# Performance work log

Hardware: AMD Instinct MI355X
Metric: run time of the kernel (lower is better)

The kernel has to match this reference:

```python
import jax, jax.numpy as jnp
import numpy as np

H = 32          # query heads
HKV = 8         # kv heads
HD = 128        # head dim
BS = 64         # sparse block size
LOCAL = 16      # local blocks
VERT = 8        # vertical stride
STEP = 1        # head sliding step = max(1, VERT // H) for non-homo heads
BASE = 1000000.0
ROPE_SCALE = 1.0
SCALE = 1.0 / np.sqrt(HD)


def setup_inputs() -> dict:
    key = jax.random.key(0)
    ks = jax.random.split(key, 6)
    T, D = 2048, H * HD
    std = 0.02
    return {
        'hidden_states': jax.random.normal(ks[0], (T, D), jnp.float32),
        'positions': jnp.arange(T, dtype=jnp.int32),
        'Wq': jax.random.normal(ks[1], (D, H * HD), jnp.float32) * std,
        'bq': jnp.zeros((H * HD,), jnp.float32),
        'Wk': jax.random.normal(ks[2], (D, HKV * HD), jnp.float32) * std,
        'bk': jnp.zeros((HKV * HD,), jnp.float32),
        'Wv': jax.random.normal(ks[3], (D, HKV * HD), jnp.float32) * std,
        'bv': jnp.zeros((HKV * HD,), jnp.float32),
        'Wo': jax.random.normal(ks[4], (D, D), jnp.float32) * std,
        'bo': jnp.zeros((D,), jnp.float32),
    }


def _rope_cos_sin(positions):
    # neox-style rotary, linear scaling (factor 1.0 -> identity)
    inv_freq = 1.0 / (BASE ** (jnp.arange(0, HD, 2, dtype=jnp.float32) / HD))  # [HD/2]
    t = positions.astype(jnp.float32) / ROPE_SCALE                             # [T]
    freqs = t[:, None] * inv_freq[None, :]                                     # [T, HD/2]
    return jnp.cos(freqs), jnp.sin(freqs)


def _apply_rope(x, cos, sin):
    # x: [T, h, HD], neox: rotate halves
    x1, x2 = x[..., : HD // 2], x[..., HD // 2 :]
    c, s = cos[:, None, :], sin[:, None, :]
    return jnp.concatenate([x1 * c - x2 * s, x2 * c + x1 * s], axis=-1)


def _block_sparse_mask(T):
    # per-head local + vertical-stride block pattern, causal at token level
    blk = jnp.arange(T) // BS
    qb, kb = blk[:, None], blk[None, :]                      # [T,T] block ids
    heads = jnp.arange(H)
    local = (qb - kb) < LOCAL                                # [T,T]
    vert = ((kb[None, :, :] + heads[:, None, None] * STEP + 1) % VERT) == 0  # [H,T,T]
    causal = jnp.arange(T)[:, None] >= jnp.arange(T)[None, :]
    return causal[None] & (local[None] | vert)               # [H,T,T] bool


def reference(hidden_states, positions, Wq, bq, Wk, bk, Wv, bv, Wo, bo):
    T = hidden_states.shape[0]
    q = (hidden_states @ Wq + bq).reshape(T, H, HD)
    k = (hidden_states @ Wk + bk).reshape(T, HKV, HD)
    v = (hidden_states @ Wv + bv).reshape(T, HKV, HD)

    cos, sin = _rope_cos_sin(positions)
    q = _apply_rope(q, cos, sin)
    k = _apply_rope(k, cos, sin)

    # GQA: repeat kv heads to match query heads
    k = jnp.repeat(k, H // HKV, axis=1)   # [T,H,HD]
    v = jnp.repeat(v, H // HKV, axis=1)

    scores = jnp.einsum('shd,thd->hst', q, k) * SCALE         # [H,T,T]
    mask = _block_sparse_mask(T)
    scores = jnp.where(mask, scores, jnp.finfo(scores.dtype).min)
    probs = jax.nn.softmax(scores, axis=-1)
    out = jnp.einsum('hst,thd->shd', probs, v).reshape(T, H * HD)
    return out @ Wo + bo
```

## Files before the change

kernel.cpp:

```cpp
#include <hip/hip_runtime.h>
#include <type_traits>

#define H_    32
#define HKV_  8
#define HD_   128
#define D_    4096
#define KVD_  1024
#define NQKV_ 6144

typedef __attribute__((ext_vector_type(8))) short s8v;
typedef __attribute__((ext_vector_type(4))) float f4v;

__device__ __forceinline__ float b2f(unsigned short u) {
  union { unsigned int i; float f; } v; v.i = ((unsigned int)u) << 16; return v.f;
}
__device__ __forceinline__ unsigned short f2b(float f) {
  unsigned int u = __float_as_uint(f);
  u += 0x7fffu + ((u >> 16) & 1u);
  return (unsigned short)(u >> 16);
}

__device__ __forceinline__ void gload16(const unsigned short* g, unsigned short* l) {
  __builtin_amdgcn_global_load_lds((const __attribute__((address_space(1))) void*)g,
                                   (__attribute__((address_space(3))) void*)l, 16, 0, 0);
}

__global__ void cvt_bf16(const float* __restrict__ x, unsigned short* __restrict__ y,
                         int n8)
{
  int i = blockIdx.x * blockDim.x + threadIdx.x;
  if (i >= n8) return;
  const float4* xp = (const float4*)x + (size_t)i * 2;
  float4 a = xp[0], b = xp[1];
  s8v v;
  v[0] = (short)f2b(a.x); v[1] = (short)f2b(a.y);
  v[2] = (short)f2b(a.z); v[3] = (short)f2b(a.w);
  v[4] = (short)f2b(b.x); v[5] = (short)f2b(b.y);
  v[6] = (short)f2b(b.z); v[7] = (short)f2b(b.w);
  *(s8v*)(y + (size_t)i * 8) = v;
}

__global__ void concat_bias(const float* __restrict__ bq, const float* __restrict__ bk,
                            const float* __restrict__ bv, float* __restrict__ o)
{
  int i = blockIdx.x * blockDim.x + threadIdx.x;
  float v = (i < D_) ? bq[i] : (i < D_ + KVD_) ? bk[i - D_] : bv[i - D_ - KVD_];
  o[i] = v;
}

__global__ __launch_bounds__(256) void cvt_transpose(
    const float* __restrict__ W, unsigned short* __restrict__ Wt, int K, int N)
{
  __shared__ unsigned short tile[64][72];
  const int k0 = blockIdx.y * 64, n0 = blockIdx.x * 64;
  const int tid = threadIdx.x;
#pragma unroll
  for (int it = 0; it < 4; ++it) {
    int idx = tid + it * 256;
    int r = idx >> 4;
    int c = (idx & 15) << 2;
    float4 w = *(const float4*)(W + (size_t)(k0 + r) * N + n0 + c);
    tile[c + 0][r] = f2b(w.x); tile[c + 1][r] = f2b(w.y);
    tile[c + 2][r] = f2b(w.z); tile[c + 3][r] = f2b(w.w);
  }
  __syncthreads();
#pragma unroll
  for (int it = 0; it < 2; ++it) {
    int idx = tid + it * 256;
    int n = idx >> 3;
    int kk = (idx & 7) << 3;
    *(s8v*)(Wt + (size_t)(n0 + n) * K + k0 + kk) = *(const s8v*)&tile[n][kk];
  }
}

__global__ __launch_bounds__(256) void vtrans(
    const unsigned short* __restrict__ S, int lds_, unsigned short* __restrict__ Dst,
    int T)
{
  __shared__ unsigned short tile[64][72];
  const int v0 = blockIdx.x * 64, t0 = blockIdx.y * 64;
  const int tid = threadIdx.x;
#pragma unroll
  for (int it = 0; it < 2; ++it) {
    int idx = tid + it * 256;
    int tr = idx >> 3;
    int vc = (idx & 7) << 3;
    s8v val = *(const s8v*)(S + (size_t)(t0 + tr) * lds_ + v0 + vc);
#pragma unroll
    for (int u = 0; u < 8; ++u) tile[vc + u][tr] = (unsigned short)val[u];
  }
  __syncthreads();
#pragma unroll
  for (int it = 0; it < 2; ++it) {
    int idx = tid + it * 256;
    int vr = idx >> 3;
    int tc = (idx & 7) << 3;
    *(s8v*)(Dst + (size_t)(v0 + vr) * T + t0 + tc) = *(const s8v*)&tile[vr][tc];
  }
}

template <typename OT>
__global__ __launch_bounds__(512, 2) void gemm_bt4p(
    const unsigned short* __restrict__ A, const unsigned short* __restrict__ Bt,
    const float* __restrict__ bias, OT* __restrict__ C,
    int M, int N, int K, int ldc)
{
  __shared__ __align__(16) unsigned short lds[65536];

  const int tid  = threadIdx.x;
  const int wave = tid >> 6;
  const int lane = tid & 63;
  const int l16  = lane & 15;
  const int quad = lane >> 4;
  const int wm   = wave >> 2;
  const int wn   = wave & 3;

  const int nbx = N >> 8;
  const int nwg = nbx * (M >> 8);
  int bid = blockIdx.x;
  if ((nwg & 7) == 0) bid = (bid & 7) * (nwg >> 3) + (bid >> 3);
  const int row0 = (bid / nbx) << 8;
  const int col0 = (bid % nbx) << 8;

  const int srow = lane >> 2;
  const int scol = (((lane & 3) ^ ((lane >> 3) & 3)) << 3);
  const unsigned short* ApL = A  + (size_t)(row0 + wave * 32 + srow) * K + scol;
  const unsigned short* BpL = Bt + (size_t)(col0 + wave * 32 + srow) * K + scol;

  unsigned short* ldsA = lds;
  unsigned short* ldsB = lds + 32768;
  const int wst = wave * 1024;

  const int sl = ((quad ^ ((l16 >> 1) & 3)) << 3);
  const int arow = wm * 128 + l16;
  const int brow = wn * 64 + l16;

  f4v acc[8][4] = {};
  const int nt = K >> 6;

  {
    const unsigned short* sa = ApL;
    const unsigned short* sb = BpL;
    gload16(sa,                       ldsA + wst);
    gload16(sa + 16 * (size_t)K,      ldsA + wst + 512);
    gload16(sb,                       ldsB + wst);
    gload16(sb + 16 * (size_t)K,      ldsB + wst + 512);
    gload16(sa + 32,                  ldsA + 8192 + wst);
    gload16(sa + 32 + 16 * (size_t)K, ldsA + 8192 + wst + 512);
    gload16(sb + 32,                  ldsB + 8192 + wst);
    gload16(sb + 32 + 16 * (size_t)K, ldsB + 8192 + wst + 512);
  }
  asm volatile("s_waitcnt vmcnt(4)" ::: "memory");
  asm volatile("s_barrier" ::: "memory");

  for (int t = 0; t < nt; ++t) {
    const int p = t & 1;
    const unsigned short* Ab0 = ldsA + p * 16384;
    const unsigned short* Ab1 = Ab0 + 8192;
    const unsigned short* Bb0 = ldsB + p * 16384;
    const unsigned short* Bb1 = Bb0 + 8192;
    unsigned short* An = ldsA + (p ^ 1) * 16384;
    unsigned short* Bn = ldsB + (p ^ 1) * 16384;
    const bool pre = (t + 1 < nt);
    const unsigned short* sa = ApL + (size_t)(t + 1) * 64;
    const unsigned short* sb = BpL + (size_t)(t + 1) * 64;

    s8v a[8], b0, b1, b2, b3;

    b0 = *(const s8v*)&Bb0[(brow +  0) * 32 + sl];
    b1 = *(const s8v*)&Bb0[(brow + 16) * 32 + sl];
#pragma unroll
    for (int i = 0; i < 8; ++i)
      a[i] = *(const s8v*)&Ab0[(arow + i * 16) * 32 + sl];
    if (pre) {
      gload16(sa,                  An + wst);
      gload16(sa + 16 * (size_t)K, An + wst + 512);
    }
    __builtin_amdgcn_s_setprio(1);
#pragma unroll
    for (int i = 0; i < 8; ++i) {
      acc[i][0] = __builtin_amdgcn_mfma_f32_16x16x32_bf16(a[i], b0, acc[i][0], 0, 0, 0);
      acc[i][1] = __builtin_amdgcn_mfma_f32_16x16x32_bf16(a[i], b1, acc[i][1], 0, 0, 0);
    }
    __builtin_amdgcn_s_setprio(0);

    b2 = *(const s8v*)&Bb0[(brow + 32) * 32 + sl];
    b3 = *(const s8v*)&Bb0[(brow + 48) * 32 + sl];
    if (pre) {
      gload16(sb,                  Bn + wst);
      gload16(sb + 16 * (size_t)K, Bn + wst + 512);
      asm volatile("s_waitcnt vmcnt(4)" ::: "memory");
    } else {
      asm volatile("s_waitcnt vmcnt(0)" ::: "memory");
    }
    asm volatile("s_barrier" ::: "memory");
    __builtin_amdgcn_s_setprio(1);
#pragma unroll
    for (int i = 0; i < 8; ++i) {
      acc[i][2] = __builtin_amdgcn_mfma_f32_16x16x32_bf16(a[i], b2, acc[i][2], 0, 0, 0);
      acc[i][3] = __builtin_amdgcn_mfma_f32_16x16x32_bf16(a[i], b3, acc[i][3], 0, 0, 0);
    }
    __builtin_amdgcn_s_setprio(0);

    b2 = *(const s8v*)&Bb1[(brow + 32) * 32 + sl];
    b3 = *(const s8v*)&Bb1[(brow + 48) * 32 + sl];
#pragma unroll
    for (int i = 0; i < 8; ++i)
      a[i] = *(const s8v*)&Ab1[(arow + i * 16) * 32 + sl];
    if (pre) {
      gload16(sa + 32,                  An + 8192 + wst);
      gload16(sa + 32 + 16 * (size_t)K, An + 8192 + wst + 512);
    }
    __builtin_amdgcn_s_setprio(1);
#pragma unroll
    for (int i = 0; i < 8; ++i) {
      acc[i][2] = __builtin_amdgcn_mfma_f32_16x16x32_bf16(a[i], b2, acc[i][2], 0, 0, 0);
      acc[i][3] = __builtin_amdgcn_mfma_f32_16x16x32_bf16(a[i], b3, acc[i][3], 0, 0, 0);
    }
    __builtin_amdgcn_s_setprio(0);

    b0 = *(const s8v*)&Bb1[(brow +  0) * 32 + sl];
    b1 = *(const s8v*)&Bb1[(brow + 16) * 32 + sl];
    if (pre) {
      gload16(sb + 32,                  Bn + 8192 + wst);
      gload16(sb + 32 + 16 * (size_t)K, Bn + 8192 + wst + 512);
      asm volatile("s_waitcnt vmcnt(4)" ::: "memory");
    }
    asm volatile("s_barrier" ::: "memory");
    __builtin_amdgcn_s_setprio(1);
#pragma unroll
    for (int i = 0; i < 8; ++i) {
      acc[i][0] = __builtin_amdgcn_mfma_f32_16x16x32_bf16(a[i], b0, acc[i][0], 0, 0, 0);
      acc[i][1] = __builtin_amdgcn_mfma_f32_16x16x32_bf16(a[i], b1, acc[i][1], 0, 0, 0);
    }
    __builtin_amdgcn_s_setprio(0);
  }

#pragma unroll
  for (int j = 0; j < 4; ++j) {
    const int col = col0 + wn * 64 + j * 16 + l16;
    const float bc = bias[col];
#pragma unroll
    for (int i = 0; i < 8; ++i) {
      const int rowb = row0 + wm * 128 + i * 16 + quad * 4;
#pragma unroll
      for (int r = 0; r < 4; ++r) {
        float o = acc[i][j][r] + bc;
        if constexpr (std::is_same_v<OT, float>) C[(size_t)(rowb + r) * ldc + col] = o;
        else                                     C[(size_t)(rowb + r) * ldc + col] = f2b(o);
      }
    }
  }
}

__global__ void sincos_tab(const int* __restrict__ pos, float* __restrict__ ct,
                           float* __restrict__ st)
{
  const int t = blockIdx.x, d = threadIdx.x;
  float inv = powf(1.0e6f, -(float)d * (1.0f / 64.0f));
  float fr  = (float)pos[t] * inv;
  float s, c;
  sincosf(fr, &s, &c);
  ct[t * 64 + d] = c;
  st[t * 64 + d] = s;
}

__global__ void rope_apply(unsigned short* __restrict__ qkv,
                           const float* __restrict__ ct, const float* __restrict__ st,
                           int T)
{
  const int t  = blockIdx.x;
  const int hh = blockIdx.y;
  const int d  = threadIdx.x;
  unsigned short* p = qkv + (size_t)t * NQKV_ + hh * HD_;
  const float g = (hh < H_) ? (0.08838834764831845f * 1.4426950408889634f) : 1.0f;
  float c = ct[t * 64 + d], s = st[t * 64 + d];
  float x1 = b2f(p[d]), x2 = b2f(p[d + 64]);
  p[d]      = f2b((x1 * c - x2 * s) * g);
  p[d + 64] = f2b((x2 * c + x1 * s) * g);
}

__global__ __launch_bounds__(256) void attn_sparse(
    const unsigned short* __restrict__ QKV, int ldq,
    const unsigned short* __restrict__ Vt, unsigned short* __restrict__ O, int T)
{
  __shared__ __align__(16) unsigned short lds[16384];
  unsigned short* ldsK = lds;
  unsigned short* ldsV = lds + 8192;
  unsigned short* ldsP = lds;

  const int h    = blockIdx.x;
  const int qb   = (gridDim.y - 1) - blockIdx.y;
  const int hkv  = h >> 2;
  const int tid  = threadIdx.x;
  const int wave = tid >> 6;
  const int lane = tid & 63;
  const int l16  = lane & 15;
  const int quad = lane >> 4;

  const int qrow = qb * 64 + wave * 16 + l16;
  s8v qf[4];
#pragma unroll
  for (int s = 0; s < 4; ++s)
    qf[s] = *(const s8v*)(QKV + (size_t)qrow * ldq + h * HD_ + s * 32 + quad * 8);

  const int lr4 = lane >> 2;
  const int lc8 = (lane & 3) << 3;
  const unsigned short* Kp0 = QKV + (size_t)(wave * 16 + lr4) * ldq
                              + D_ + hkv * HD_ + lc8;
  unsigned short* Kd0 = ldsK + wave * 512;
  const unsigned short* Vp0 = Vt + (size_t)(hkv * HD_ + wave * 32 + lr4) * T + lc8;
  unsigned short* Vd0 = ldsV + wave * 1024;

  float mrow[4] = {-1e30f, -1e30f, -1e30f, -1e30f};
  float lrow[4] = {0.f, 0.f, 0.f, 0.f};
  f4v oacc[8] = {};
  const int rowinb = wave * 16 + quad * 4;

  for (int kb = 0; kb <= qb; ++kb) {
    if (!((qb - kb < 16) || (((kb + h + 1) & 7) == 0))) continue;

    __syncthreads();
    {
      const unsigned short* kp = Kp0 + (size_t)(kb * 64) * ldq;
      const unsigned short* vp = Vp0 + kb * 64;
#pragma unroll
      for (int t = 0; t < 4; ++t)
        gload16(kp + t * 32, Kd0 + t * 2048);
#pragma unroll
      for (int t = 0; t < 4; ++t)
        gload16(vp + (size_t)((t >> 1) * 16) * T + (t & 1) * 32,
                Vd0 + (t & 1) * 4096 + (t >> 1) * 512);
    }
    __syncthreads();

    f4v sacc[4] = {};
#pragma unroll
    for (int kt = 0; kt < 4; ++kt) {
#pragma unroll
      for (int s = 0; s < 4; ++s) {
        s8v b = *(const s8v*)&ldsK[s * 2048 + (kt * 16 + l16) * 32 + quad * 8];
        sacc[kt] = __builtin_amdgcn_mfma_f32_16x16x32_bf16(qf[s], b, sacc[kt], 0, 0, 0);
      }
    }
    __syncthreads();

    const bool diag = (kb == qb);
    float p[4][4];
#pragma unroll
    for (int r = 0; r < 4; ++r) {
      float mx = -1e30f;
#pragma unroll
      for (int kt = 0; kt < 4; ++kt) {
        float sc = sacc[kt][r];
        if (diag && (kt * 16 + l16 > rowinb + r)) sc = -1e30f;
        p[r][kt] = sc;
        mx = fmaxf(mx, sc);
      }
#pragma unroll
      for (int off = 1; off < 16; off <<= 1)
        mx = fmaxf(mx, __shfl_xor(mx, off));
      float newm = fmaxf(mrow[r], mx);
      float alpha = exp2f(mrow[r] - newm);
      mrow[r] = newm;
      float rs = 0.f;
#pragma unroll
      for (int kt = 0; kt < 4; ++kt) {
        unsigned short pb = f2b(exp2f(p[r][kt] - newm));
        ldsP[wave * 1152 + (quad * 4 + r) * 72 + kt * 16 + l16] = pb;
        rs += b2f(pb);
      }
#pragma unroll
      for (int off = 1; off < 16; off <<= 1)
        rs += __shfl_xor(rs, off);
      lrow[r] = lrow[r] * alpha + rs;
#pragma unroll
      for (int dt = 0; dt < 8; ++dt) oacc[dt][r] *= alpha;
    }

#pragma unroll
    for (int s2 = 0; s2 < 2; ++s2) {
      s8v af = *(const s8v*)&ldsP[wave * 1152 + l16 * 72 + s2 * 32 + quad * 8];
#pragma unroll
      for (int dt = 0; dt < 8; ++dt) {
        s8v vf = *(const s8v*)&ldsV[s2 * 4096 + (dt * 16 + l16) * 32 + quad * 8];
        oacc[dt] = __builtin_amdgcn_mfma_f32_16x16x32_bf16(af, vf, oacc[dt], 0, 0, 0);
      }
    }
  }

#pragma unroll
  for (int r = 0; r < 4; ++r) {
    float inv = 1.0f / lrow[r];
    size_t rowoff = (size_t)(qb * 64 + rowinb + r) * D_ + h * HD_;
#pragma unroll
    for (int dt = 0; dt < 8; ++dt)
      O[rowoff + dt * 16 + l16] = f2b(oacc[dt][r] * inv);
  }
}

extern "C" void kernel_launch(void* const* d_in, const int* in_sizes, int n_in,
                              void* d_out, int out_size, void* d_ws, size_t ws_size,
                              hipStream_t stream)
{
  const float* hs  = (const float*)d_in[0];
  const int*   pos = (const int*)d_in[1];
  const float* Wq  = (const float*)d_in[2];
  const float* bq  = (const float*)d_in[3];
  const float* Wk  = (const float*)d_in[4];
  const float* bk  = (const float*)d_in[5];
  const float* Wv  = (const float*)d_in[6];
  const float* bv  = (const float*)d_in[7];
  const float* Wo  = (const float*)d_in[8];
  const float* bo  = (const float*)d_in[9];
  float* out = (float*)d_out;

  const int T = in_sizes[1];

  const size_t nQ = (size_t)T * D_;
  unsigned short* hsb  = (unsigned short*)d_ws;
  unsigned short* qkv  = hsb + nQ;
  unsigned short* vt   = qkv + (size_t)T * NQKV_;
  unsigned short* wbuf = vt  + (size_t)KVD_ * T;
  unsigned short* tail = wbuf + (size_t)NQKV_ * D_;
  float* bqkv = (float*)tail;
  float* ct   = bqkv + NQKV_;
  float* st   = ct + (size_t)T * 64;
  unsigned short* abuf = hsb;

  dim3 blk(256);
  cvt_bf16<<<dim3((int)(nQ / 8 / 256)), blk, 0, stream>>>(hs, hsb, (int)(nQ / 8));
  concat_bias<<<dim3(NQKV_ / 256), blk, 0, stream>>>(bq, bk, bv, bqkv);
  sincos_tab<<<dim3(T), dim3(64), 0, stream>>>(pos, ct, st);

  cvt_transpose<<<dim3(D_ / 64,   D_ / 64), blk, 0, stream>>>(Wq, wbuf, D_, D_);
  cvt_transpose<<<dim3(KVD_ / 64, D_ / 64), blk, 0, stream>>>(
      Wk, wbuf + (size_t)D_ * D_, D_, KVD_);
  cvt_transpose<<<dim3(KVD_ / 64, D_ / 64), blk, 0, stream>>>(
      Wv, wbuf + (size_t)(D_ + KVD_) * D_, D_, KVD_);

  gemm_bt4p<unsigned short><<<dim3((NQKV_ / 256) * (T / 256)), dim3(512), 0, stream>>>(
      hsb, wbuf, bqkv, qkv, T, NQKV_, D_, NQKV_);

  rope_apply<<<dim3(T, H_ + HKV_), dim3(64), 0, stream>>>(qkv, ct, st, T);
  vtrans<<<dim3(KVD_ / 64, T / 64), blk, 0, stream>>>(
      qkv + D_ + KVD_, NQKV_, vt, T);

  attn_sparse<<<dim3(H_, T / 64), blk, 0, stream>>>(qkv, NQKV_, vt, abuf, T);

  cvt_transpose<<<dim3(D_ / 64, D_ / 64), blk, 0, stream>>>(Wo, wbuf, D_, D_);
  gemm_bt4p<float><<<dim3((D_ / 256) * (T / 256)), dim3(512), 0, stream>>>(
      abuf, wbuf, bo, out, T, D_, D_, D_);
}
```

Baseline: 509.7 us.

## Use dedicated 128x128-tile GEMM for output projection to improve CU occupancy

Replaces the 256x256-tile GEMM used for the output projection with a new 128x128-tile kernel using 256 threads and two blocks per CU. This raises the workgroup count from 128 to 512 for the 2048x4096 output, so the GPU's many CUs are better filled. The new kernel has its own double-buffered LDS pipeline with interleaved loads and MFMA, and XCD-aware block remapping. In exchange, each tile gets less operand reuse, so more global and LDS traffic per FLOP.

```diff
diff --git a/kernel.cpp b/kernel.cpp
--- a/kernel.cpp
+++ b/kernel.cpp
@@ -253,6 +253,156 @@
   }
 }
 
+__global__ __launch_bounds__(256, 2) void gemm_o128(
+    const unsigned short* __restrict__ A, const unsigned short* __restrict__ Bt,
+    const float* __restrict__ bias, float* __restrict__ C,
+    int M, int N, int K)
+{
+  __shared__ __align__(16) unsigned short lds[32768];
+
+  const int tid  = threadIdx.x;
+  const int wave = tid >> 6;
+  const int lane = tid & 63;
+  const int l16  = lane & 15;
+  const int quad = lane >> 4;
+  const int wm   = wave >> 1;
+  const int wn   = wave & 1;
+
+  const int nbx = N >> 7;
+  const int nwg = nbx * (M >> 7);
+  int bid = blockIdx.x;
+  if ((nwg & 7) == 0) bid = (bid & 7) * (nwg >> 3) + (bid >> 3);
+  const int row0 = (bid / nbx) << 7;
+  const int col0 = (bid % nbx) << 7;
+
+  const int srow = lane >> 2;
+  const int scol = (((lane & 3) ^ ((lane >> 3) & 3)) << 3);
+  const unsigned short* ApL = A  + (size_t)(row0 + wave * 16 + srow) * K + scol;
+  const unsigned short* BpL = Bt + (size_t)(col0 + wave * 16 + srow) * K + scol;
+
+  unsigned short* ldsA = lds;
+  unsigned short* ldsB = lds + 16384;
+  const int wst = wave * 512;
+
+  const int sl = ((quad ^ ((l16 >> 1) & 3)) << 3);
+  const int arow = wm * 64 + l16;
+  const int brow = wn * 64 + l16;
+
+  f4v acc[4][4] = {};
+  const int nt = K >> 6;
+
+  {
+    const unsigned short* sa = ApL;
+    const unsigned short* sb = BpL;
+    gload16(sa,                       ldsA + wst);
+    gload16(sa + 64 * (size_t)K,      ldsA + wst + 2048);
+    gload16(sb,                       ldsB + wst);
+    gload16(sb + 64 * (size_t)K,      ldsB + wst + 2048);
+    gload16(sa + 32,                  ldsA + 4096 + wst);
+    gload16(sa + 32 + 64 * (size_t)K, ldsA + 4096 + wst + 2048);
+    gload16(sb + 32,                  ldsB + 4096 + wst);
+    gload16(sb + 32 + 64 * (size_t)K, ldsB + 4096 + wst + 2048);
+  }
+  asm volatile("s_waitcnt vmcnt(4)" ::: "memory");
+  asm volatile("s_barrier" ::: "memory");
+
+  for (int t = 0; t < nt; ++t) {
+    const int p = t & 1;
+    const unsigned short* Ab0 = ldsA + p * 8192;
+    const unsigned short* Ab1 = Ab0 + 4096;
+    const unsigned short* Bb0 = ldsB + p * 8192;
+    const unsigned short* Bb1 = Bb0 + 4096;
+    unsigned short* An = ldsA + (p ^ 1) * 8192;
+    unsigned short* Bn = ldsB + (p ^ 1) * 8192;
+    const bool pre = (t + 1 < nt);
+    const unsigned short* sa = ApL + (size_t)(t + 1) * 64;
+    const unsigned short* sb = BpL + (size_t)(t + 1) * 64;
+
+    s8v a[4], b0, b1, b2, b3;
+
+    b0 = *(const s8v*)&Bb0[(brow +  0) * 32 + sl];
+    b1 = *(const s8v*)&Bb0[(brow + 16) * 32 + sl];
+#pragma unroll
+    for (int i = 0; i < 4; ++i)
+      a[i] = *(const s8v*)&Ab0[(arow + i * 16) * 32 + sl];
+    if (pre) {
+      gload16(sa,                  An + wst);
+      gload16(sa + 64 * (size_t)K, An + wst + 2048);
+    }
+    __builtin_amdgcn_s_setprio(1);
+#pragma unroll
+    for (int i = 0; i < 4; ++i) {
+      acc[i][0] = __builtin_amdgcn_mfma_f32_16x16x32_bf16(a[i], b0, acc[i][0], 0, 0, 0);
+      acc[i][1] = __builtin_amdgcn_mfma_f32_16x16x32_bf16(a[i], b1, acc[i][1], 0, 0, 0);
+    }
+    __builtin_amdgcn_s_setprio(0);
+
+    b2 = *(const s8v*)&Bb0[(brow + 32) * 32 + sl];
+    b3 = *(const s8v*)&Bb0[(brow + 48) * 32 + sl];
+    if (pre) {
+      gload16(sb,                  Bn + wst);
+      gload16(sb + 64 * (size_t)K, Bn + wst + 2048);
+      asm volatile("s_waitcnt vmcnt(4)" ::: "memory");
+    } else {
+      asm volatile("s_waitcnt vmcnt(0)" ::: "memory");
+    }
+    asm volatile("s_barrier" ::: "memory");
+    __builtin_amdgcn_s_setprio(1);
+#pragma unroll
+    for (int i = 0; i < 4; ++i) {
+      acc[i][2] = __builtin_amdgcn_mfma_f32_16x16x32_bf16(a[i], b2, acc[i][2], 0, 0, 0);
+      acc[i][3] = __builtin_amdgcn_mfma_f32_16x16x32_bf16(a[i], b3, acc[i][3], 0, 0, 0);
+    }
+    __builtin_amdgcn_s_setprio(0);
+
+    b2 = *(const s8v*)&Bb1[(brow + 32) * 32 + sl];
+    b3 = *(const s8v*)&Bb1[(brow + 48) * 32 + sl];
+#pragma unroll
+    for (int i = 0; i < 4; ++i)
+      a[i] = *(const s8v*)&Ab1[(arow + i * 16) * 32 + sl];
+    if (pre) {
+      gload16(sa + 32,                  An + 4096 + wst);
+      gload16(sa + 32 + 64 * (size_t)K, An + 4096 + wst + 2048);
+    }
+    __builtin_amdgcn_s_setprio(1);
+#pragma unroll
+    for (int i = 0; i < 4; ++i) {
+      acc[i][2] = __builtin_amdgcn_mfma_f32_16x16x32_bf16(a[i], b2, acc[i][2], 0, 0, 0);
+      acc[i][3] = __builtin_amdgcn_mfma_f32_16x16x32_bf16(a[i], b3, acc[i][3], 0, 0, 0);
+    }
+    __builtin_amdgcn_s_setprio(0);
+
+    b0 = *(const s8v*)&Bb1[(brow +  0) * 32 + sl];
+    b1 = *(const s8v*)&Bb1[(brow + 16) * 32 + sl];
+    if (pre) {
+      gload16(sb + 32,                  Bn + 4096 + wst);
+      gload16(sb + 32 + 64 * (size_t)K, Bn + 4096 + wst + 2048);
+      asm volatile("s_waitcnt vmcnt(4)" ::: "memory");
+    }
+    asm volatile("s_barrier" ::: "memory");
+    __builtin_amdgcn_s_setprio(1);
+#pragma unroll
+    for (int i = 0; i < 4; ++i) {
+      acc[i][0] = __builtin_amdgcn_mfma_f32_16x16x32_bf16(a[i], b0, acc[i][0], 0, 0, 0);
+      acc[i][1] = __builtin_amdgcn_mfma_f32_16x16x32_bf16(a[i], b1, acc[i][1], 0, 0, 0);
+    }
+    __builtin_amdgcn_s_setprio(0);
+  }
+
+#pragma unroll
+  for (int j = 0; j < 4; ++j) {
+    const int col = col0 + wn * 64 + j * 16 + l16;
+    const float bc = bias[col];
+#pragma unroll
+    for (int i = 0; i < 4; ++i) {
+      const int rowb = row0 + wm * 64 + i * 16 + quad * 4;
+#pragma unroll
+      for (int r = 0; r < 4; ++r)
+        C[(size_t)(rowb + r) * N + col] = acc[i][j][r] + bc;
+    }
+  }
+}
+
 __global__ void sincos_tab(const int* __restrict__ pos, float* __restrict__ ct,
                            float* __restrict__ st)
 {
@@ -449,6 +599,6 @@
   attn_sparse<<<dim3(H_, T / 64), blk, 0, stream>>>(qkv, NQKV_, vt, abuf, T);
 
   cvt_transpose<<<dim3(D_ / 64, D_ / 64), blk, 0, stream>>>(Wo, wbuf, D_, D_);
-  gemm_bt4p<float><<<dim3((D_ / 256) * (T / 256)), dim3(512), 0, stream>>>(
-      abuf, wbuf, bo, out, T, D_, D_, D_);
-}
+  gemm_o128<<<dim3((D_ / 128) * (T / 128)), dim3(256), 0, stream>>>(
+      abuf, wbuf, bo, out, T, D_, D_);
+}
```

Result: no change. 518.2 us (+1.7%).

## Add 256x128-tile output projection GEMM and vectorize RoPE application

Applied to the files above, without the earlier changes.

Adds a dedicated output-projection GEMM that uses 256x128 tiles, which doubles the workgroup count for the 2048x4096 output. It keeps a double-buffered split-K LDS pipeline with XCD-aware block remapping and raised wave priority around the MFMA sections. The RoPE kernel now uses one block per token with 8-wide vector loads and stores instead of scalar per-element work. Smaller tiles improve occupancy across the CUs but lower per-tile data reuse, which adds global and LDS traffic per FLOP.

```diff
diff --git a/kernel.cpp b/kernel.cpp
--- a/kernel.cpp
+++ b/kernel.cpp
@@ -253,6 +253,124 @@
   }
 }
 
+__global__ __launch_bounds__(512, 1) void gemm_on(
+    const unsigned short* __restrict__ A, const unsigned short* __restrict__ Bt,
+    const float* __restrict__ bias, float* __restrict__ C,
+    int M, int N, int K)
+{
+  __shared__ __align__(16) unsigned short lds[49152];
+
+  const int tid  = threadIdx.x;
+  const int wave = tid >> 6;
+  const int lane = tid & 63;
+  const int l16  = lane & 15;
+  const int quad = lane >> 4;
+  const int wm   = wave >> 2;
+  const int wn   = wave & 3;
+
+  const int nbx = N >> 7;
+  const int nwg = nbx * (M >> 8);
+  int bid = blockIdx.x;
+  if ((nwg & 7) == 0) bid = (bid & 7) * (nwg >> 3) + (bid >> 3);
+  const int row0 = (bid / nbx) << 8;
+  const int col0 = (bid % nbx) << 7;
+
+  const int srow = lane >> 2;
+  const int scol = (((lane & 3) ^ ((lane >> 3) & 3)) << 3);
+  const unsigned short* ApL = A  + (size_t)(row0 + wave * 32 + srow) * K + scol;
+  const unsigned short* BpL = Bt + (size_t)(col0 + wave * 16 + srow) * K + scol;
+
+  unsigned short* ldsA = lds;
+  unsigned short* ldsB = lds + 32768;
+  const int wstA = wave * 1024;
+  const int wstB = wave * 512;
+
+  const int sl = ((quad ^ ((l16 >> 1) & 3)) << 3);
+  const int arow = wm * 128 + l16;
+  const int brow = wn * 32 + l16;
+
+  f4v acc[8][2] = {};
+  const int nt = K >> 6;
+
+  gload16(ApL,                       ldsA + wstA);
+  gload16(ApL + 16 * (size_t)K,      ldsA + wstA + 512);
+  gload16(BpL,                       ldsB + wstB);
+  gload16(ApL + 32,                  ldsA + 8192 + wstA);
+  gload16(ApL + 32 + 16 * (size_t)K, ldsA + 8192 + wstA + 512);
+  gload16(BpL + 32,                  ldsB + 4096 + wstB);
+  asm volatile("s_waitcnt vmcnt(3)" ::: "memory");
+  asm volatile("s_barrier" ::: "memory");
+
+  for (int t = 0; t < nt; ++t) {
+    const int p = t & 1;
+    const unsigned short* Ab0 = ldsA + p * 16384;
+    const unsigned short* Ab1 = Ab0 + 8192;
+    const unsigned short* Bb0 = ldsB + p * 8192;
+    const unsigned short* Bb1 = Bb0 + 4096;
+    unsigned short* An = ldsA + (p ^ 1) * 16384;
+    unsigned short* Bn = ldsB + (p ^ 1) * 8192;
+    const bool pre = (t + 1 < nt);
+    const unsigned short* sa = ApL + (size_t)(t + 1) * 64;
+    const unsigned short* sb = BpL + (size_t)(t + 1) * 64;
+
+    s8v a[8], b0, b1;
+
+    b0 = *(const s8v*)&Bb0[(brow +  0) * 32 + sl];
+    b1 = *(const s8v*)&Bb0[(brow + 16) * 32 + sl];
+#pragma unroll
+    for (int i = 0; i < 8; ++i)
+      a[i] = *(const s8v*)&Ab0[(arow + i * 16) * 32 + sl];
+    if (pre) {
+      gload16(sa,                  An + wstA);
+      gload16(sa + 16 * (size_t)K, An + wstA + 512);
+      gload16(sb,                  Bn + wstB);
+    }
+    __builtin_amdgcn_s_setprio(1);
+#pragma unroll
+    for (int i = 0; i < 8; ++i) {
+      acc[i][0] = __builtin_amdgcn_mfma_f32_16x16x32_bf16(a[i], b0, acc[i][0], 0, 0, 0);
+      acc[i][1] = __builtin_amdgcn_mfma_f32_16x16x32_bf16(a[i], b1, acc[i][1], 0, 0, 0);
+    }
+    __builtin_amdgcn_s_setprio(0);
+    if (pre) { asm volatile("s_waitcnt vmcnt(3)" ::: "memory"); }
+    else     { asm volatile("s_waitcnt vmcnt(0)" ::: "memory"); }
+    asm volatile("s_barrier" ::: "memory");
+
+    b0 = *(const s8v*)&Bb1[(brow +  0) * 32 + sl];
+    b1 = *(const s8v*)&Bb1[(brow + 16) * 32 + sl];
+#pragma unroll
+    for (int i = 0; i < 8; ++i)
+      a[i] = *(const s8v*)&Ab1[(arow + i * 16) * 32 + sl];
+    if (pre) {
+      gload16(sa + 32,                  An + 8192 + wstA);
+      gload16(sa + 32 + 16 * (size_t)K, An + 8192 + wstA + 512);
+      gload16(sb + 32,                  Bn + 4096 + wstB);
+    }
+    __builtin_amdgcn_s_setprio(1);
+#pragma unroll
+    for (int i = 0; i < 8; ++i) {
+      acc[i][0] = __builtin_amdgcn_mfma_f32_16x16x32_bf16(a[i], b0, acc[i][0], 0, 0, 0);
+      acc[i][1] = __builtin_amdgcn_mfma_f32_16x16x32_bf16(a[i], b1, acc[i][1], 0, 0, 0);
+    }
+    __builtin_amdgcn_s_setprio(0);
+    if (pre) { asm volatile("s_waitcnt vmcnt(3)" ::: "memory"); }
+    asm volatile("s_barrier" ::: "memory");
+  }
+
+#pragma unroll
+  for (int j = 0; j < 2; ++j) {
+    const int col = col0 + wn * 32 + j * 16 + l16;
+    const float bc = bias[col];
+#pragma unroll
+    for (int i = 0; i < 8; ++i) {
+      const int rowb = row0 + wm * 128 + i * 16 + quad * 4;
+#pragma unroll
+      for (int r = 0; r < 4; ++r)
+        C[(size_t)(rowb + r) * N + col] = acc[i][j][r] + bc;
+    }
+  }
+}
+
 __global__ void sincos_tab(const int* __restrict__ pos, float* __restrict__ ct,
                            float* __restrict__ st)
 {
@@ -265,19 +383,35 @@
   st[t * 64 + d] = s;
 }
 
-__global__ void rope_apply(unsigned short* __restrict__ qkv,
-                           const float* __restrict__ ct, const float* __restrict__ st,
-                           int T)
-{
-  const int t  = blockIdx.x;
-  const int hh = blockIdx.y;
-  const int d  = threadIdx.x;
+__global__ __launch_bounds__(320) void rope_apply2(
+    unsigned short* __restrict__ qkv,
+    const float* __restrict__ ct, const float* __restrict__ st, int T)
+{
+  const int t   = blockIdx.x;
+  const int tid = threadIdx.x;
+  const int hh  = tid >> 3;
+  const int d0  = (tid & 7) << 3;
   unsigned short* p = qkv + (size_t)t * NQKV_ + hh * HD_;
   const float g = (hh < H_) ? (0.08838834764831845f * 1.4426950408889634f) : 1.0f;
-  float c = ct[t * 64 + d], s = st[t * 64 + d];
-  float x1 = b2f(p[d]), x2 = b2f(p[d + 64]);
-  p[d]      = f2b((x1 * c - x2 * s) * g);
-  p[d + 64] = f2b((x2 * c + x1 * s) * g);
+
+  s8v x1 = *(const s8v*)(p + d0);
+  s8v x2 = *(const s8v*)(p + 64 + d0);
+  const float4* cp = (const float4*)(ct + t * 64 + d0);
+  const float4* sp = (const float4*)(st + t * 64 + d0);
+  float4 ca = cp[0], cb = cp[1], sa = sp[0], sb = sp[1];
+  float cc[8] = {ca.x, ca.y, ca.z, ca.w, cb.x, cb.y, cb.z, cb.w};
+  float ss[8] = {sa.x, sa.y, sa.z, sa.w, sb.x, sb.y, sb.z, sb.w};
+
+  s8v o1, o2;
+#pragma unroll
+  for (int u = 0; u < 8; ++u) {
+    float a = b2f((unsigned short)x1[u]);
+    float b = b2f((unsigned short)x2[u]);
+    o1[u] = (short)f2b((a * cc[u] - b * ss[u]) * g);
+    o2[u] = (short)f2b((b * cc[u] + a * ss[u]) * g);
+  }
+  *(s8v*)(p + d0)      = o1;
+  *(s8v*)(p + 64 + d0) = o2;
 }
 
 __global__ __launch_bounds__(256) void attn_sparse(
@@ -442,13 +576,13 @@
   gemm_bt4p<unsigned short><<<dim3((NQKV_ / 256) * (T / 256)), dim3(512), 0, stream>>>(
       hsb, wbuf, bqkv, qkv, T, NQKV_, D_, NQKV_);
 
-  rope_apply<<<dim3(T, H_ + HKV_), dim3(64), 0, stream>>>(qkv, ct, st, T);
+  rope_apply2<<<dim3(T), dim3(320), 0, stream>>>(qkv, ct, st, T);
   vtrans<<<dim3(KVD_ / 64, T / 64), blk, 0, stream>>>(
       qkv + D_ + KVD_, NQKV_, vt, T);
 
   attn_sparse<<<dim3(H_, T / 64), blk, 0, stream>>>(qkv, NQKV_, vt, abuf, T);
 
   cvt_transpose<<<dim3(D_ / 64, D_ / 64), blk, 0, stream>>>(Wo, wbuf, D_, D_);
-  gemm_bt4p<float><<<dim3((D_ / 256) * (T / 256)), dim3(512), 0, stream>>>(
-      abuf, wbuf, bo, out, T, D_, D_, D_);
-}
+  gemm_on<<<dim3((D_ / 128) * (T / 256)), dim3(512), 0, stream>>>(
+      abuf, wbuf, bo, out, T, D_, D_);
+}
```

Result: faster. 495.8 us (-2.7%).
